# Optimization experiments

Measured on AMD Instinct MI355X. Metric: run time of the kernel, lower is better.

Reference implementation:

```python
import jax, jax.numpy as jnp
import numpy as np

B, LQ, LK = 8, 2048, 2048
DQ = DK = DI = DV = 1024
SCALE = 1.0 / np.sqrt(DK).astype(np.float32)  # (sqrt(1/sqrt(dk)))^2 applied to q and k
NEG_INF = float('-inf')


def setup_inputs() -> dict:
    key = jax.random.key(0)
    ks = jax.random.split(key, 6)
    return {
        'query': jax.random.normal(ks[0], (B, LQ, DQ), dtype=jnp.float32),
        'key': jax.random.normal(ks[1], (B, LK, DK), dtype=jnp.float32),
        'value': jax.random.normal(ks[2], (B, LK, DV), dtype=jnp.float32),
        'mask': jax.random.randint(ks[3], (B, 1, LK), 0, 2, dtype=jnp.int32),
        'Wq': jax.random.normal(ks[4], (DI, DQ), dtype=jnp.float32) / np.sqrt(DQ),
        'Wk': jax.random.normal(ks[5], (DI, DK), dtype=jnp.float32) / np.sqrt(DK),
    }


def reference(query, key, value, mask, Wq, Wk):
    # Linear projections (bias=False): y = x @ W^T
    q = jnp.einsum('bld,ed->ble', query, Wq)           # [B,LQ,DI]
    k = jnp.einsum('bld,ed->ble', key, Wk)             # [B,LK,DI]
    scores = jnp.einsum('bqe,bke->bqk', q, k) * SCALE  # [B,LQ,LK]
    scores = scores.astype(jnp.float32)
    scores = jnp.where(mask == 0, NEG_INF, scores)     # mask broadcasts [B,1,LK]
    attn_weight = jax.nn.softmax(scores, axis=-1)      # fp32 softmax, dropout p=0 -> identity
    attn_cxt = jnp.einsum('bqk,bkd->bqd', attn_weight, value)
    return attn_cxt, attn_weight
```

## Files before the change

### kernel.cpp

```cpp
#include <hip/hip_runtime.h>


typedef __bf16 bf16x8 __attribute__((ext_vector_type(8)));
typedef float  f32x4  __attribute__((ext_vector_type(4)));

#define AS1 __attribute__((address_space(1)))
#define AS3 __attribute__((address_space(3)))

__device__ __forceinline__ ushort f2bf(float f) {
  union { float f; unsigned u; } v; v.f = f;
  unsigned u = v.u;
  unsigned r = (u + 0x7FFFu + ((u >> 16) & 1u)) >> 16;
  return (ushort)r;
}

constexpr float SCORE_SCALE = 0.03125f;

template <int MODE>
__global__ __launch_bounds__(256, 2)
void gemm_bt(const ushort* __restrict__ Ag, const ushort* __restrict__ Bg,
             void* __restrict__ Cv, const int* __restrict__ mask,
             int N, int K, long sA, long sB, long sC, int sMask)
{
  __shared__ ushort As[128 * 64];
  __shared__ ushort Bs[128 * 64];

  const int b = blockIdx.z;
  const ushort* Ab = Ag + (long)b * sA;
  const ushort* Bb = Bg + (long)b * sB;

  const int tid  = threadIdx.x;
  const int lane = tid & 63;
  const int wid  = tid >> 6;
  const int wr   = wid >> 1;
  const int wc   = wid & 1;
  const int m0   = blockIdx.y * 128;
  const int n0   = blockIdx.x * 128;

  const int srow = lane >> 3;
  const int skof = (lane & 7) * 8;

  const int laneQuad = lane >> 4;
  const int lane15   = lane & 15;
  const int fko      = laneQuad * 8;

  f32x4 acc[4][4];
#pragma unroll
  for (int i = 0; i < 4; ++i)
#pragma unroll
    for (int j = 0; j < 4; ++j) acc[i][j] = (f32x4){0.f, 0.f, 0.f, 0.f};

  for (int kt = 0; kt < K; kt += 64) {
#pragma unroll
    for (int r = 0; r < 4; ++r) {
      const int rowblk = (r * 4 + wid) * 8;
      const ushort* ga = Ab + (long)(m0 + rowblk + srow) * K + (kt + skof);
      __builtin_amdgcn_global_load_lds((const AS1 void*)ga,
                                       (AS3 void*)(As + rowblk * 64), 16, 0, 0);
      const ushort* gb = Bb + (long)(n0 + rowblk + srow) * K + (kt + skof);
      __builtin_amdgcn_global_load_lds((const AS1 void*)gb,
                                       (AS3 void*)(Bs + rowblk * 64), 16, 0, 0);
    }
    __syncthreads();

#pragma unroll
    for (int kk = 0; kk < 64; kk += 32) {
      bf16x8 af[4], bfr[4];
#pragma unroll
      for (int mi = 0; mi < 4; ++mi)
        af[mi] = *(const bf16x8*)(As + (wr * 64 + mi * 16 + lane15) * 64 + kk + fko);
#pragma unroll
      for (int ni = 0; ni < 4; ++ni)
        bfr[ni] = *(const bf16x8*)(Bs + (wc * 64 + ni * 16 + lane15) * 64 + kk + fko);
#pragma unroll
      for (int mi = 0; mi < 4; ++mi)
#pragma unroll
        for (int ni = 0; ni < 4; ++ni)
          acc[mi][ni] = __builtin_amdgcn_mfma_f32_16x16x32_bf16(
              af[mi], bfr[ni], acc[mi][ni], 0, 0, 0);
    }
    __syncthreads();
  }

  const int rbase = laneQuad * 4;
  if constexpr (MODE == 0) {
    ushort* C = (ushort*)Cv + (long)b * sC;
#pragma unroll
    for (int mi = 0; mi < 4; ++mi) {
      const int r0 = m0 + wr * 64 + mi * 16 + rbase;
#pragma unroll
      for (int ni = 0; ni < 4; ++ni) {
        const int col = n0 + wc * 64 + ni * 16 + lane15;
#pragma unroll
        for (int r = 0; r < 4; ++r)
          C[(long)(r0 + r) * N + col] = f2bf(acc[mi][ni][r]);
      }
    }
  } else if constexpr (MODE == 1) {
    float* C = (float*)Cv + (long)b * sC;
    const int* mb = mask + (long)b * sMask;
    int   mk[4]; int coln[4];
#pragma unroll
    for (int ni = 0; ni < 4; ++ni) {
      coln[ni] = n0 + wc * 64 + ni * 16 + lane15;
      mk[ni]   = mb[coln[ni]];
    }
    const float ninf = -__builtin_inff();
#pragma unroll
    for (int mi = 0; mi < 4; ++mi) {
      const int r0 = m0 + wr * 64 + mi * 16 + rbase;
#pragma unroll
      for (int ni = 0; ni < 4; ++ni)
#pragma unroll
        for (int r = 0; r < 4; ++r)
          C[(long)(r0 + r) * N + coln[ni]] =
              mk[ni] ? acc[mi][ni][r] * SCORE_SCALE : ninf;
    }
  } else {
    float* C = (float*)Cv + (long)b * sC;
#pragma unroll
    for (int mi = 0; mi < 4; ++mi) {
      const int r0 = m0 + wr * 64 + mi * 16 + rbase;
#pragma unroll
      for (int ni = 0; ni < 4; ++ni) {
        const int col = n0 + wc * 64 + ni * 16 + lane15;
#pragma unroll
        for (int r = 0; r < 4; ++r)
          C[(long)(r0 + r) * N + col] = acc[mi][ni][r];
      }
    }
  }
}

__global__ __launch_bounds__(256)
void cvt_f32_bf16(const float* __restrict__ in, ushort* __restrict__ out, int n4)
{
  const int i = blockIdx.x * 256 + threadIdx.x;
  if (i >= n4) return;
  float4 v = ((const float4*)in)[i];
  ushort4 o;
  o.x = f2bf(v.x); o.y = f2bf(v.y); o.z = f2bf(v.z); o.w = f2bf(v.w);
  ((ushort4*)out)[i] = o;
}

__global__ __launch_bounds__(256)
void transpose_v(const float* __restrict__ V, ushort* __restrict__ Vt)
{
  __shared__ ushort t[64][65];
  const int b = blockIdx.z;
  const float* Vb  = V  + (long)b * 2048 * 1024;
  ushort*      Vtb = Vt + (long)b * 1024 * 2048;
  const int k0 = blockIdx.x * 64, d0 = blockIdx.y * 64;
  const int c  = threadIdx.x & 63;
  const int r4 = threadIdx.x >> 6;
#pragma unroll
  for (int i = 0; i < 64; i += 4)
    t[i + r4][c] = f2bf(Vb[(long)(k0 + i + r4) * 1024 + d0 + c]);
  __syncthreads();
#pragma unroll
  for (int i = 0; i < 64; i += 4)
    Vtb[(long)(d0 + i + r4) * 2048 + k0 + c] = t[c][i + r4];
}

__global__ __launch_bounds__(256)
void softmax_rows(float* __restrict__ S, ushort* __restrict__ Wb)
{
  const long row = blockIdx.x;
  float*  Sr = S  + row * 2048;
  ushort* Wr = Wb + row * 2048;
  const int tid = threadIdx.x;

  float4 a = *(const float4*)(Sr + tid * 4);
  float4 c = *(const float4*)(Sr + 1024 + tid * 4);

  float m = fmaxf(fmaxf(fmaxf(a.x, a.y), fmaxf(a.z, a.w)),
                  fmaxf(fmaxf(c.x, c.y), fmaxf(c.z, c.w)));
#pragma unroll
  for (int off = 32; off > 0; off >>= 1) m = fmaxf(m, __shfl_xor(m, off, 64));

  __shared__ float red[8];
  const int wid = tid >> 6, lane = tid & 63;
  if (lane == 0) red[wid] = m;
  __syncthreads();
  m = fmaxf(fmaxf(red[0], red[1]), fmaxf(red[2], red[3]));

  float e[8];
  e[0] = __expf(a.x - m); e[1] = __expf(a.y - m);
  e[2] = __expf(a.z - m); e[3] = __expf(a.w - m);
  e[4] = __expf(c.x - m); e[5] = __expf(c.y - m);
  e[6] = __expf(c.z - m); e[7] = __expf(c.w - m);
  float s = e[0] + e[1] + e[2] + e[3] + e[4] + e[5] + e[6] + e[7];
#pragma unroll
  for (int off = 32; off > 0; off >>= 1) s += __shfl_xor(s, off, 64);
  if (lane == 0) red[4 + wid] = s;
  __syncthreads();
  s = red[4] + red[5] + red[6] + red[7];

  const float inv = 1.0f / s;
  float4 o0 = make_float4(e[0] * inv, e[1] * inv, e[2] * inv, e[3] * inv);
  float4 o1 = make_float4(e[4] * inv, e[5] * inv, e[6] * inv, e[7] * inv);
  *(float4*)(Sr + tid * 4)        = o0;
  *(float4*)(Sr + 1024 + tid * 4) = o1;
  ushort4 w0, w1;
  w0.x = f2bf(o0.x); w0.y = f2bf(o0.y); w0.z = f2bf(o0.z); w0.w = f2bf(o0.w);
  w1.x = f2bf(o1.x); w1.y = f2bf(o1.y); w1.z = f2bf(o1.z); w1.w = f2bf(o1.w);
  *(ushort4*)(Wr + tid * 4)        = w0;
  *(ushort4*)(Wr + 1024 + tid * 4) = w1;
}

constexpr size_t SZ_XB  = 16384UL * 1024 * 2;
constexpr size_t OFF_QB = 0;
constexpr size_t OFF_KB = SZ_XB;
constexpr size_t OFF_WQ = 2 * SZ_XB;
constexpr size_t OFF_WK = OFF_WQ + 1024UL * 1024 * 2;
constexpr size_t OFF_QP = OFF_WK + 1024UL * 1024 * 2;
constexpr size_t OFF_KP = OFF_QP + SZ_XB;
constexpr size_t OFF_VT = OFF_KP + SZ_XB;
constexpr size_t OFF_WB = 0;

extern "C" void kernel_launch(void* const* d_in, const int* in_sizes, int n_in,
                              void* d_out, int out_size, void* d_ws, size_t ws_size,
                              hipStream_t stream)
{
  (void)in_sizes; (void)n_in; (void)out_size; (void)ws_size;

  const float* query = (const float*)d_in[0];
  const float* key   = (const float*)d_in[1];
  const float* value = (const float*)d_in[2];
  const int*   mask  = (const int*)d_in[3];
  const float* Wq    = (const float*)d_in[4];
  const float* Wk    = (const float*)d_in[5];

  float* out_cxt = (float*)d_out;
  float* out_w   = out_cxt + 8L * 2048 * 1024;

  char* ws = (char*)d_ws;
  ushort* qb  = (ushort*)(ws + OFF_QB);
  ushort* kb  = (ushort*)(ws + OFF_KB);
  ushort* wqb = (ushort*)(ws + OFF_WQ);
  ushort* wkb = (ushort*)(ws + OFF_WK);
  ushort* Qp  = (ushort*)(ws + OFF_QP);
  ushort* Kp  = (ushort*)(ws + OFF_KP);
  ushort* Vt  = (ushort*)(ws + OFF_VT);
  ushort* Wb  = (ushort*)(ws + OFF_WB);

  cvt_f32_bf16<<<16384, 256, 0, stream>>>(query, qb, 4194304);
  cvt_f32_bf16<<<16384, 256, 0, stream>>>(key,   kb, 4194304);
  cvt_f32_bf16<<<1024,  256, 0, stream>>>(Wq, wqb, 262144);
  cvt_f32_bf16<<<1024,  256, 0, stream>>>(Wk, wkb, 262144);
  transpose_v<<<dim3(32, 16, 8), 256, 0, stream>>>(value, Vt);

  gemm_bt<0><<<dim3(8, 128, 1), 256, 0, stream>>>(qb, wqb, Qp, nullptr,
                                                  1024, 1024, 0, 0, 0, 0);
  gemm_bt<0><<<dim3(8, 128, 1), 256, 0, stream>>>(kb, wkb, Kp, nullptr,
                                                  1024, 1024, 0, 0, 0, 0);

  gemm_bt<1><<<dim3(16, 16, 8), 256, 0, stream>>>(Qp, Kp, out_w, mask,
                                                  2048, 1024,
                                                  2048L * 1024, 2048L * 1024,
                                                  2048L * 2048, 2048);

  softmax_rows<<<16384, 256, 0, stream>>>(out_w, Wb);

  gemm_bt<2><<<dim3(8, 16, 8), 256, 0, stream>>>(Wb, Vt, out_cxt, nullptr,
                                                 1024, 2048,
                                                 2048L * 2048, 1024L * 2048,
                                                 2048L * 1024, 0);
}
```

Baseline: 713.3 us.

## Rewrite GEMM with 256x256 tiles, double-buffered LDS, swizzle and XCD remap

The shared bf16 GEMM kernel now uses 512-thread blocks with 256x256 output tiles. It double-buffers LDS so global-to-LDS loads for the next K tile overlap with MFMA on the current one, and it XOR-swizzles LDS columns to avoid bank conflicts. Workgroup IDs are remapped so consecutive tiles land on the same XCD for better L2 reuse, and s_setprio is raised around the MFMA bursts. The larger tiles need 128 KB LDS per block and more accumulator registers, which may limit occupancy and leave fewer blocks to fill the CUs on the smaller grids.

```diff
diff --git a/kernel.cpp b/kernel.cpp
--- a/kernel.cpp
+++ b/kernel.cpp
@@ -17,98 +17,147 @@
 constexpr float SCORE_SCALE = 0.03125f;
 
 template <int MODE>
-__global__ __launch_bounds__(256, 2)
+__global__ __launch_bounds__(512, 2)
 void gemm_bt(const ushort* __restrict__ Ag, const ushort* __restrict__ Bg,
              void* __restrict__ Cv, const int* __restrict__ mask,
              int N, int K, long sA, long sB, long sC, int sMask)
 {
-  __shared__ ushort As[128 * 64];
-  __shared__ ushort Bs[128 * 64];
-
-  const int b = blockIdx.z;
-  const ushort* Ab = Ag + (long)b * sA;
-  const ushort* Bb = Bg + (long)b * sB;
+  __shared__ ushort As[2][256 * 64];
+  __shared__ ushort Bs[2][256 * 64];
+
+  const int nx = gridDim.x, ny = gridDim.y, nz = gridDim.z;
+  const long nwg = (long)nx * ny * nz;
+  long flat = blockIdx.x + (long)nx * (blockIdx.y + (long)ny * blockIdx.z);
+  int bx = blockIdx.x, by = blockIdx.y, bz = blockIdx.z;
+  if ((nwg & 7) == 0) {
+    const long cpx = nwg >> 3;
+    flat = (flat & 7) * cpx + (flat >> 3);
+    bx = (int)(flat % nx);
+    by = (int)((flat / nx) % ny);
+    bz = (int)(flat / ((long)nx * ny));
+  }
+  const int m0 = by * 256;
+  const int n0 = bx * 256;
+
+  const ushort* Ab = Ag + (long)bz * sA;
+  const ushort* Bb = Bg + (long)bz * sB;
 
   const int tid  = threadIdx.x;
   const int lane = tid & 63;
   const int wid  = tid >> 6;
-  const int wr   = wid >> 1;
-  const int wc   = wid & 1;
-  const int m0   = blockIdx.y * 128;
-  const int n0   = blockIdx.x * 128;
-
-  const int srow = lane >> 3;
-  const int skof = (lane & 7) * 8;
-
-  const int laneQuad = lane >> 4;
-  const int lane15   = lane & 15;
-  const int fko      = laneQuad * 8;
-
-  f32x4 acc[4][4];
-#pragma unroll
-  for (int i = 0; i < 4; ++i)
+  const int wm   = wid >> 2;
+  const int wn   = wid & 3;
+  const int l15  = lane & 15;
+  const int lq   = lane >> 4;
+
+  long gAoff[4], gBoff[4];
+  int  ldsoff[4];
+#pragma unroll
+  for (int j = 0; j < 4; ++j) {
+    const int idx = j * 512 + tid;
+    const int row = idx >> 3;
+    const int lc  = (idx & 7) ^ (row & 7);
+    gAoff[j]  = (long)(m0 + row) * K + lc * 8;
+    gBoff[j]  = (long)(n0 + row) * K + lc * 8;
+    ldsoff[j] = (j * 512 + wid * 64) * 8;
+  }
+
+  f32x4 acc[8][4];
+#pragma unroll
+  for (int i = 0; i < 8; ++i)
 #pragma unroll
     for (int j = 0; j < 4; ++j) acc[i][j] = (f32x4){0.f, 0.f, 0.f, 0.f};
 
-  for (int kt = 0; kt < K; kt += 64) {
-#pragma unroll
-    for (int r = 0; r < 4; ++r) {
-      const int rowblk = (r * 4 + wid) * 8;
-      const ushort* ga = Ab + (long)(m0 + rowblk + srow) * K + (kt + skof);
-      __builtin_amdgcn_global_load_lds((const AS1 void*)ga,
-                                       (AS3 void*)(As + rowblk * 64), 16, 0, 0);
-      const ushort* gb = Bb + (long)(n0 + rowblk + srow) * K + (kt + skof);
-      __builtin_amdgcn_global_load_lds((const AS1 void*)gb,
-                                       (AS3 void*)(Bs + rowblk * 64), 16, 0, 0);
-    }
-    __syncthreads();
-
-#pragma unroll
-    for (int kk = 0; kk < 64; kk += 32) {
-      bf16x8 af[4], bfr[4];
-#pragma unroll
-      for (int mi = 0; mi < 4; ++mi)
-        af[mi] = *(const bf16x8*)(As + (wr * 64 + mi * 16 + lane15) * 64 + kk + fko);
-#pragma unroll
-      for (int ni = 0; ni < 4; ++ni)
-        bfr[ni] = *(const bf16x8*)(Bs + (wc * 64 + ni * 16 + lane15) * 64 + kk + fko);
-#pragma unroll
-      for (int mi = 0; mi < 4; ++mi)
+  const int nt = K >> 6;
+
+#pragma unroll
+  for (int j = 0; j < 4; ++j)
+    __builtin_amdgcn_global_load_lds((const AS1 void*)(Ab + gAoff[j]),
+                                     (AS3 void*)(&As[0][ldsoff[j]]), 16, 0, 0);
+#pragma unroll
+  for (int j = 0; j < 4; ++j)
+    __builtin_amdgcn_global_load_lds((const AS1 void*)(Bb + gBoff[j]),
+                                     (AS3 void*)(&Bs[0][ldsoff[j]]), 16, 0, 0);
+
+  const int arow0 = wm * 128 + l15;
+  const int brow0 = wn * 64 + l15;
+
+  for (int t = 0; t < nt; ++t) {
+    const ushort* Abuf = As[t & 1];
+    const ushort* Bbuf = Bs[t & 1];
+
+    if (t + 1 < nt) {
+      const long ko = (long)(t + 1) * 64;
+      const int  nb = (t + 1) & 1;
+#pragma unroll
+      for (int j = 0; j < 4; ++j)
+        __builtin_amdgcn_global_load_lds((const AS1 void*)(Ab + gAoff[j] + ko),
+                                         (AS3 void*)(&As[nb][ldsoff[j]]), 16, 0, 0);
+#pragma unroll
+      for (int j = 0; j < 4; ++j)
+        __builtin_amdgcn_global_load_lds((const AS1 void*)(Bb + gBoff[j] + ko),
+                                         (AS3 void*)(&Bs[nb][ldsoff[j]]), 16, 0, 0);
+      asm volatile("s_waitcnt vmcnt(8)" ::: "memory");
+    } else {
+      asm volatile("s_waitcnt vmcnt(0)" ::: "memory");
+    }
+    __builtin_amdgcn_sched_barrier(0);
+    __builtin_amdgcn_s_barrier();
+    __builtin_amdgcn_sched_barrier(0);
+
+#pragma unroll
+    for (int kk = 0; kk < 2; ++kk) {
+      bf16x8 bfr[4];
+#pragma unroll
+      for (int ni = 0; ni < 4; ++ni) {
+        const int row = brow0 + ni * 16;
+        const int pc  = (kk * 4 + lq) ^ (row & 7);
+        bfr[ni] = *(const bf16x8*)(Bbuf + row * 64 + pc * 8);
+      }
+      __builtin_amdgcn_s_setprio(1);
+#pragma unroll
+      for (int mi = 0; mi < 8; ++mi) {
+        const int row = arow0 + mi * 16;
+        const int pc  = (kk * 4 + lq) ^ (row & 7);
+        const bf16x8 a = *(const bf16x8*)(Abuf + row * 64 + pc * 8);
 #pragma unroll
         for (int ni = 0; ni < 4; ++ni)
           acc[mi][ni] = __builtin_amdgcn_mfma_f32_16x16x32_bf16(
-              af[mi], bfr[ni], acc[mi][ni], 0, 0, 0);
-    }
-    __syncthreads();
+              a, bfr[ni], acc[mi][ni], 0, 0, 0);
+      }
+      __builtin_amdgcn_s_setprio(0);
+    }
+    __builtin_amdgcn_sched_barrier(0);
+    __builtin_amdgcn_s_barrier();
   }
 
-  const int rbase = laneQuad * 4;
+  const int rbase = lq * 4;
   if constexpr (MODE == 0) {
-    ushort* C = (ushort*)Cv + (long)b * sC;
-#pragma unroll
-    for (int mi = 0; mi < 4; ++mi) {
-      const int r0 = m0 + wr * 64 + mi * 16 + rbase;
+    ushort* C = (ushort*)Cv + (long)bz * sC;
+#pragma unroll
+    for (int mi = 0; mi < 8; ++mi) {
+      const int r0 = m0 + wm * 128 + mi * 16 + rbase;
 #pragma unroll
       for (int ni = 0; ni < 4; ++ni) {
-        const int col = n0 + wc * 64 + ni * 16 + lane15;
+        const int col = n0 + wn * 64 + ni * 16 + l15;
 #pragma unroll
         for (int r = 0; r < 4; ++r)
           C[(long)(r0 + r) * N + col] = f2bf(acc[mi][ni][r]);
       }
     }
   } else if constexpr (MODE == 1) {
-    float* C = (float*)Cv + (long)b * sC;
-    const int* mb = mask + (long)b * sMask;
-    int   mk[4]; int coln[4];
+    float* C = (float*)Cv + (long)bz * sC;
+    const int* mb = mask + (long)bz * sMask;
+    int coln[4], mk[4];
 #pragma unroll
     for (int ni = 0; ni < 4; ++ni) {
-      coln[ni] = n0 + wc * 64 + ni * 16 + lane15;
+      coln[ni] = n0 + wn * 64 + ni * 16 + l15;
       mk[ni]   = mb[coln[ni]];
     }
     const float ninf = -__builtin_inff();
 #pragma unroll
-    for (int mi = 0; mi < 4; ++mi) {
-      const int r0 = m0 + wr * 64 + mi * 16 + rbase;
+    for (int mi = 0; mi < 8; ++mi) {
+      const int r0 = m0 + wm * 128 + mi * 16 + rbase;
 #pragma unroll
       for (int ni = 0; ni < 4; ++ni)
 #pragma unroll
@@ -117,13 +166,13 @@
               mk[ni] ? acc[mi][ni][r] * SCORE_SCALE : ninf;
     }
   } else {
-    float* C = (float*)Cv + (long)b * sC;
-#pragma unroll
-    for (int mi = 0; mi < 4; ++mi) {
-      const int r0 = m0 + wr * 64 + mi * 16 + rbase;
+    float* C = (float*)Cv + (long)bz * sC;
+#pragma unroll
+    for (int mi = 0; mi < 8; ++mi) {
+      const int r0 = m0 + wm * 128 + mi * 16 + rbase;
 #pragma unroll
       for (int ni = 0; ni < 4; ++ni) {
-        const int col = n0 + wc * 64 + ni * 16 + lane15;
+        const int col = n0 + wn * 64 + ni * 16 + l15;
 #pragma unroll
         for (int r = 0; r < 4; ++r)
           C[(long)(r0 + r) * N + col] = acc[mi][ni][r];
@@ -250,20 +299,20 @@
   cvt_f32_bf16<<<1024,  256, 0, stream>>>(Wk, wkb, 262144);
   transpose_v<<<dim3(32, 16, 8), 256, 0, stream>>>(value, Vt);
 
-  gemm_bt<0><<<dim3(8, 128, 1), 256, 0, stream>>>(qb, wqb, Qp, nullptr,
-                                                  1024, 1024, 0, 0, 0, 0);
-  gemm_bt<0><<<dim3(8, 128, 1), 256, 0, stream>>>(kb, wkb, Kp, nullptr,
-                                                  1024, 1024, 0, 0, 0, 0);
-
-  gemm_bt<1><<<dim3(16, 16, 8), 256, 0, stream>>>(Qp, Kp, out_w, mask,
-                                                  2048, 1024,
-                                                  2048L * 1024, 2048L * 1024,
-                                                  2048L * 2048, 2048);
+  gemm_bt<0><<<dim3(4, 64, 1), 512, 0, stream>>>(qb, wqb, Qp, nullptr,
+                                                 1024, 1024, 0, 0, 0, 0);
+  gemm_bt<0><<<dim3(4, 64, 1), 512, 0, stream>>>(kb, wkb, Kp, nullptr,
+                                                 1024, 1024, 0, 0, 0, 0);
+
+  gemm_bt<1><<<dim3(8, 8, 8), 512, 0, stream>>>(Qp, Kp, out_w, mask,
+                                                2048, 1024,
+                                                2048L * 1024, 2048L * 1024,
+                                                2048L * 2048, 2048);
 
   softmax_rows<<<16384, 256, 0, stream>>>(out_w, Wb);
 
-  gemm_bt<2><<<dim3(8, 16, 8), 256, 0, stream>>>(Wb, Vt, out_cxt, nullptr,
-                                                 1024, 2048,
-                                                 2048L * 2048, 1024L * 2048,
-                                                 2048L * 1024, 0);
-}
+  gemm_bt<2><<<dim3(4, 8, 8), 512, 0, stream>>>(Wb, Vt, out_cxt, nullptr,
+                                                1024, 2048,
+                                                2048L * 2048, 1024L * 2048,
+                                                2048L * 1024, 0);
+}
```

Result: faster. 640.4 us (-10.2%).
